# Performance work log

Measured on AMD Instinct MI355X. Metric: run time of the kernel, lower is better.

Reference implementation:

```python
import jax, jax.numpy as jnp
import numpy as np

B, D, H = 16384, 1024, 1024


def setup_inputs() -> dict:
    key = jax.random.key(0)
    ks = jax.random.split(key, 6)
    s = 1.0 / np.sqrt(D)
    return {
        "x": jax.random.normal(ks[0], (B, D), jnp.float32),
        "h_prev": jax.random.normal(ks[1], (B, H), jnp.float32),
        "c_prev": jax.random.normal(ks[2], (B, H), jnp.float32),
        "dynamic_weight": jax.random.uniform(ks[3], (B, H), jnp.float32),
        # stacked gate weights: order [i, f, o, c, s] along first axis
        "Wx": jax.random.normal(ks[4], (5 * H, D), jnp.float32) * s,
        "bx": jnp.zeros((5 * H,), jnp.float32),
        "Uh": jax.random.normal(ks[5], (5 * H, H), jnp.float32) * s,
        "bh": jnp.zeros((5 * H,), jnp.float32),
    }


def reference(x, h_prev, c_prev, dynamic_weight, Wx, bx, Uh, bh):
    # two fused GEMMs covering all 10 original nn.Linear calls
    gates = (jnp.einsum('bd,gd->bg', x, Wx) + bx
             + jnp.einsum('bh,gh->bg', h_prev, Uh) + bh)  # [B, 5H]
    gi, gf, go, gc, gs = jnp.split(gates, 5, axis=-1)
    i_t = jax.nn.sigmoid(gi)
    f_t = jax.nn.sigmoid(gf)
    o_t = jax.nn.sigmoid(go)
    c_hat = jnp.tanh(gc)
    s_t = jax.nn.sigmoid(gs) * dynamic_weight
    c_t = f_t * c_prev + i_t * c_hat * s_t
    h_t = o_t * jnp.tanh(c_t)
    return h_t, c_t
```

## Files before the change

kernel.cpp:

```cpp
#include <hip/hip_runtime.h>
#include <hip/hip_bf16.h>

#define B_ROWS 16384
#define KDIM   2048
#define NDIM   5120
#define HDIM   1024

#define BM 256
#define BN 256
#define BK 32
#define NK (KDIM / BK)
#define BUFSZ 32768
#define NBUF  4
#define LDS_BYTES (NBUF * BUFSZ)

typedef __attribute__((ext_vector_type(8))) short short8;
typedef __attribute__((ext_vector_type(4))) float f32x4;

__device__ __forceinline__ void async_cp16(const void* g, void* l) {
  __builtin_amdgcn_global_load_lds(
      (const __attribute__((address_space(1))) void*)g,
      (__attribute__((address_space(3))) void*)l,
      16, 0, 0);
}

__global__ void detect_dtype(const unsigned short* __restrict__ p, int* flag) {
  __shared__ int cnt;
  if (threadIdx.x == 0) cnt = 0;
  __syncthreads();
  int h = 0;
  for (int i = threadIdx.x; i < 2048; i += 256) {
    int e = (p[i] >> 7) & 0xFF;
    if (e >= 137) h++;
  }
  atomicAdd(&cnt, h);
  __syncthreads();
  if (threadIdx.x == 0) *flag = (cnt >= 4) ? 1 : 0;
}

__global__ void pack_pair_f32(const float* __restrict__ s0, const float* __restrict__ s1,
                              __hip_bfloat16* __restrict__ dst, const int* __restrict__ flag,
                              long rbase, long total) {
  if (*flag == 0) return;
  long idx = ((long)blockIdx.x * blockDim.x + threadIdx.x) * 8;
  if (idx >= total) return;
  int  k = (int)(idx & (KDIM - 1));
  long r = (idx >> 11) + rbase;
  const float* s = (k < 1024) ? (s0 + r * 1024 + k) : (s1 + r * 1024 + (k - 1024));
  float4 v0 = ((const float4*)s)[0];
  float4 v1 = ((const float4*)s)[1];
  union { short8 v; __hip_bfloat16 e[8]; } u;
  u.e[0] = __float2bfloat16(v0.x); u.e[1] = __float2bfloat16(v0.y);
  u.e[2] = __float2bfloat16(v0.z); u.e[3] = __float2bfloat16(v0.w);
  u.e[4] = __float2bfloat16(v1.x); u.e[5] = __float2bfloat16(v1.y);
  u.e[6] = __float2bfloat16(v1.z); u.e[7] = __float2bfloat16(v1.w);
  *(short8*)(dst + idx) = u.v;
}

__global__ __launch_bounds__(512, 2) void gemm_bt256(
    const __hip_bfloat16* __restrict__ Abf, const __hip_bfloat16* __restrict__ Wbf,
    const void* __restrict__ xr, const void* __restrict__ hr,
    const void* __restrict__ Wxr, const void* __restrict__ Uhr,
    __hip_bfloat16* __restrict__ G, const int* __restrict__ flag, int row_base) {
  extern __shared__ char lds[];

  const int tid = threadIdx.x;
  const int w   = tid >> 6;
  const int l   = tid & 63;

  const int m0l = blockIdx.y * BM;
  const int n0  = blockIdx.x * BN;

  const int wm = w >> 2;
  const int wn = w & 3;

  const int fl = *flag;
  const __hip_bfloat16* pA[2];
  const __hip_bfloat16* pW[2];
  long dA, dW;
  {
    const int r0 = w * 32 + (l >> 2);
#pragma unroll
    for (int i = 0; i < 2; ++i) {
      const int sr = r0 + i * 16;
      const int dc = (l & 3) ^ ((sr >> 1) & 3);
      if (fl) {
        pA[i] = Abf + (long)(m0l + sr) * KDIM + dc * 8;
        pW[i] = Wbf + (long)(n0 + sr) * KDIM + dc * 8;
      } else {
        pA[i] = (const __hip_bfloat16*)xr  + (long)(row_base + m0l + sr) * 1024 + dc * 8;
        pW[i] = (const __hip_bfloat16*)Wxr + (long)(n0 + sr) * 1024 + dc * 8;
      }
    }
    if (fl) { dA = 1024; dW = 1024; }
    else {
      dA = (const __hip_bfloat16*)hr  - (const __hip_bfloat16*)xr;
      dW = (const __hip_bfloat16*)Uhr - (const __hip_bfloat16*)Wxr;
    }
  }

#define STAGE(T) do {                                                        \
    const int  b_  = (T) & 3;                                                \
    const int  k0_ = (T) * BK;                                               \
    const long ko_ = (k0_ < 1024) ? (long)k0_ : (dA + (k0_ - 1024));         \
    const long kw_ = (k0_ < 1024) ? (long)k0_ : (dW + (k0_ - 1024));         \
    char* la_ = lds + b_ * BUFSZ + w * 2048;                                 \
    char* lw_ = la_ + 16384;                                                 \
    _Pragma("unroll")                                                        \
    for (int i_ = 0; i_ < 2; ++i_) {                                         \
      async_cp16(pA[i_] + ko_, la_ + i_ * 1024);                             \
      async_cp16(pW[i_] + kw_, lw_ + i_ * 1024);                             \
    }                                                                        \
  } while (0)

  f32x4 acc[8][4] = {};
  const int frow  = l & 15;
  const int swz   = (((l >> 4) ^ ((frow >> 1) & 3)) << 4);
  const int arow0 = wm * 128 + frow;
  const int brow0 = wn * 64 + frow;

#define COMPUTE(T) do {                                                      \
    const char* ba_ = lds + ((T) & 3) * BUFSZ;                               \
    const char* bw_ = ba_ + 16384;                                           \
    short8 af_[8], wf_[4];                                                   \
    _Pragma("unroll")                                                        \
    for (int mi = 0; mi < 8; ++mi)                                           \
      af_[mi] = *(const short8*)(ba_ + (arow0 + mi * 16) * 64 + swz);        \
    _Pragma("unroll")                                                        \
    for (int ni = 0; ni < 4; ++ni)                                           \
      wf_[ni] = *(const short8*)(bw_ + (brow0 + ni * 16) * 64 + swz);        \
    __builtin_amdgcn_s_setprio(1);                                           \
    _Pragma("unroll")                                                        \
    for (int mi = 0; mi < 8; ++mi)                                           \
      _Pragma("unroll")                                                      \
      for (int ni = 0; ni < 4; ++ni)                                         \
        acc[mi][ni] = __builtin_amdgcn_mfma_f32_16x16x32_bf16(               \
            af_[mi], wf_[ni], acc[mi][ni], 0, 0, 0);                         \
    __builtin_amdgcn_s_setprio(0);                                           \
  } while (0)

  STAGE(0); STAGE(1); STAGE(2);

  int t = 0;
  for (; t < NK - 3; ++t) {
    __builtin_amdgcn_s_barrier();
    __builtin_amdgcn_sched_barrier(0);
    STAGE(t + 3);
    asm volatile("s_waitcnt vmcnt(12)" ::: "memory");
    __builtin_amdgcn_s_barrier();
    __builtin_amdgcn_sched_barrier(0);
    COMPUTE(t);
  }
  for (; t < NK; ++t) {
    __builtin_amdgcn_s_barrier();
    __builtin_amdgcn_sched_barrier(0);
    asm volatile("s_waitcnt vmcnt(0)" ::: "memory");
    __builtin_amdgcn_s_barrier();
    __builtin_amdgcn_sched_barrier(0);
    COMPUTE(t);
  }

#undef STAGE
#undef COMPUTE

  const int c_col = l & 15;
  const int c_row = (l >> 4) * 4;
#pragma unroll
  for (int mi = 0; mi < 8; ++mi) {
#pragma unroll
    for (int r = 0; r < 4; ++r) {
      long m = (long)(m0l + wm * 128 + mi * 16 + c_row + r);
      __hip_bfloat16* gp = G + m * NDIM + n0 + wn * 64 + c_col;
#pragma unroll
      for (int ni = 0; ni < 4; ++ni)
        gp[ni * 16] = __float2bfloat16(acc[mi][ni][r]);
    }
  }
}

__global__ __launch_bounds__(256, 2) void gemm_bt128(
    const __hip_bfloat16* __restrict__ Abf, const __hip_bfloat16* __restrict__ Wbf,
    const void* __restrict__ xr, const void* __restrict__ hr,
    const void* __restrict__ Wxr, const void* __restrict__ Uhr,
    __hip_bfloat16* __restrict__ G, const int* __restrict__ flag, int row_base) {
  __shared__ __hip_bfloat16 As[128 * 64];
  __shared__ __hip_bfloat16 Ws[128 * 64];

  const int tid  = threadIdx.x;
  const int wave = tid >> 6;
  const int lane = tid & 63;

  const int m0l = blockIdx.y * 128;
  const int n0  = blockIdx.x * 128;

  const int wm = (wave >> 1) * 64;
  const int wn = (wave & 1) * 64;

  const int srl  = m0l + wave * 32 + (lane >> 3);
  const int srw  = n0  + wave * 32 + (lane >> 3);
  const int scol = (lane & 7) * 8;

  const int fl = *flag;
  const __hip_bfloat16 *pA0, *pA1, *pW0, *pW1;
  long rsA, rsW;
  if (fl) {
    pA0 = Abf + (long)srl * KDIM + scol; pA1 = pA0 + 1024; rsA = KDIM;
    pW0 = Wbf + (long)srw * KDIM + scol; pW1 = pW0 + 1024; rsW = KDIM;
  } else {
    pA0 = (const __hip_bfloat16*)xr  + (long)(row_base + srl) * 1024 + scol;
    pA1 = (const __hip_bfloat16*)hr  + (long)(row_base + srl) * 1024 + scol;
    pW0 = (const __hip_bfloat16*)Wxr + (long)srw * 1024 + scol;
    pW1 = (const __hip_bfloat16*)Uhr + (long)srw * 1024 + scol;
    rsA = 1024; rsW = 1024;
  }

  __hip_bfloat16* a_l = As + (wave * 32) * 64;
  __hip_bfloat16* w_l = Ws + (wave * 32) * 64;

  f32x4 acc[4][4] = {};
  const int frow = lane & 15;
  const int fk   = (lane >> 4) * 8;

  for (int k0 = 0; k0 < KDIM; k0 += 64) {
    const __hip_bfloat16* ag = (k0 < 1024) ? pA0 + k0 : pA1 + (k0 - 1024);
    const __hip_bfloat16* wg = (k0 < 1024) ? pW0 + k0 : pW1 + (k0 - 1024);
    __syncthreads();
#pragma unroll
    for (int i = 0; i < 4; ++i) {
      async_cp16(ag + (long)i * 8 * rsA, a_l + i * 8 * 64);
      async_cp16(wg + (long)i * 8 * rsW, w_l + i * 8 * 64);
    }
    __syncthreads();
#pragma unroll
    for (int kk = 0; kk < 64; kk += 32) {
      short8 af[4], wf[4];
#pragma unroll
      for (int mi = 0; mi < 4; ++mi)
        af[mi] = *(const short8*)(As + (wm + mi * 16 + frow) * 64 + kk + fk);
#pragma unroll
      for (int ni = 0; ni < 4; ++ni)
        wf[ni] = *(const short8*)(Ws + (wn + ni * 16 + frow) * 64 + kk + fk);
#pragma unroll
      for (int mi = 0; mi < 4; ++mi)
#pragma unroll
        for (int ni = 0; ni < 4; ++ni)
          acc[mi][ni] = __builtin_amdgcn_mfma_f32_16x16x32_bf16(
              af[mi], wf[ni], acc[mi][ni], 0, 0, 0);
    }
  }

  const int c_col = lane & 15;
  const int c_row = (lane >> 4) * 4;
#pragma unroll
  for (int mi = 0; mi < 4; ++mi) {
#pragma unroll
    for (int r = 0; r < 4; ++r) {
      long m = (long)(m0l + wm + mi * 16 + c_row + r);
      __hip_bfloat16* gp = G + m * NDIM + n0 + wn + c_col;
#pragma unroll
      for (int ni = 0; ni < 4; ++ni)
        gp[ni * 16] = __float2bfloat16(acc[mi][ni][r]);
    }
  }
}

__global__ void lstm_ep(const __hip_bfloat16* __restrict__ G,
                        const void* __restrict__ cpr, const void* __restrict__ dwr,
                        const void* __restrict__ bxr, const void* __restrict__ bhr,
                        float* __restrict__ out, const int* __restrict__ flag,
                        long row_base, long rows) {
  const long t = ((long)blockIdx.x * blockDim.x + threadIdx.x) * 8;
  if (t >= rows * HDIM) return;
  const long bl = t >> 10;
  const int  h  = (int)(t & 1023);
  const long ig = (row_base + bl) * HDIM + h;

  const int fl = *flag;
  const __hip_bfloat16* g = G + bl * (long)NDIM + h;

  union S8 { short8 v; __hip_bfloat16 e[8]; };
  union F8 { float4 v[2]; float f[8]; };

  S8 vg[5];
  F8 bias[5];
#pragma unroll
  for (int q = 0; q < 5; ++q) {
    vg[q].v = *(const short8*)(g + q * 1024);
    if (fl) {
      bias[q].v[0] = *(const float4*)((const float*)bxr + q * 1024 + h);
      bias[q].v[1] = *(const float4*)((const float*)bxr + q * 1024 + h + 4);
      F8 b2;
      b2.v[0] = *(const float4*)((const float*)bhr + q * 1024 + h);
      b2.v[1] = *(const float4*)((const float*)bhr + q * 1024 + h + 4);
#pragma unroll
      for (int j = 0; j < 8; ++j) bias[q].f[j] += b2.f[j];
    } else {
      S8 b1, b2;
      b1.v = *(const short8*)((const __hip_bfloat16*)bxr + q * 1024 + h);
      b2.v = *(const short8*)((const __hip_bfloat16*)bhr + q * 1024 + h);
#pragma unroll
      for (int j = 0; j < 8; ++j)
        bias[q].f[j] = __bfloat162float(b1.e[j]) + __bfloat162float(b2.e[j]);
    }
  }

  F8 cp, dv;
  if (fl) {
    cp.v[0] = *(const float4*)((const float*)cpr + ig);
    cp.v[1] = *(const float4*)((const float*)cpr + ig + 4);
    dv.v[0] = *(const float4*)((const float*)dwr + ig);
    dv.v[1] = *(const float4*)((const float*)dwr + ig + 4);
  } else {
    S8 c8, d8;
    c8.v = *(const short8*)((const __hip_bfloat16*)cpr + ig);
    d8.v = *(const short8*)((const __hip_bfloat16*)dwr + ig);
#pragma unroll
    for (int j = 0; j < 8; ++j) {
      cp.f[j] = __bfloat162float(c8.e[j]);
      dv.f[j] = __bfloat162float(d8.e[j]);
    }
  }

  F8 oh, oc;
#pragma unroll
  for (int j = 0; j < 8; ++j) {
    float gi = __bfloat162float(vg[0].e[j]) + bias[0].f[j];
    float gf = __bfloat162float(vg[1].e[j]) + bias[1].f[j];
    float go = __bfloat162float(vg[2].e[j]) + bias[2].f[j];
    float gc = __bfloat162float(vg[3].e[j]) + bias[3].f[j];
    float gs = __bfloat162float(vg[4].e[j]) + bias[4].f[j];
    float it = 1.f / (1.f + __expf(-gi));
    float ft = 1.f / (1.f + __expf(-gf));
    float ot = 1.f / (1.f + __expf(-go));
    float ch = tanhf(gc);
    float st = (1.f / (1.f + __expf(-gs))) * dv.f[j];
    float ct = ft * cp.f[j] + it * ch * st;
    oh.f[j] = ot * tanhf(ct);
    oc.f[j] = ct;
  }
  *(float4*)(out + ig)     = oh.v[0];
  *(float4*)(out + ig + 4) = oh.v[1];
  float* oc_p = out + (long)B_ROWS * HDIM + ig;
  *(float4*)(oc_p)     = oc.v[0];
  *(float4*)(oc_p + 4) = oc.v[1];
}

extern "C" void kernel_launch(void* const* d_in, const int* in_sizes, int n_in,
                              void* d_out, int out_size, void* d_ws, size_t ws_size,
                              hipStream_t stream) {
  const void* x      = d_in[0];
  const void* h_prev = d_in[1];
  const void* c_prev = d_in[2];
  const void* dw     = d_in[3];
  const void* Wx     = d_in[4];
  const void* bx     = d_in[5];
  const void* Uh     = d_in[6];
  const void* bh     = d_in[7];

  static int lds_attr_done = 0;
  if (!lds_attr_done) {
    hipFuncSetAttribute((const void*)gemm_bt256,
                        hipFuncAttributeMaxDynamicSharedMemorySize, LDS_BYTES);
    lds_attr_done = 1;
  }

  const size_t wbf_bytes = (size_t)NDIM * KDIM * 2;
  int nc = 32;
  for (int c = 1; c <= 32; c <<= 1) {
    size_t need = 256 + wbf_bytes
                + (size_t)(B_ROWS / c) * KDIM * 2
                + (size_t)(B_ROWS / c) * NDIM * 2;
    if (need <= ws_size) { nc = c; break; }
  }
  const long rows = B_ROWS / nc;

  char* ws = (char*)d_ws;
  int* flag = (int*)ws;
  __hip_bfloat16* Wbf = (__hip_bfloat16*)(ws + 256);
  __hip_bfloat16* Abf = (__hip_bfloat16*)(ws + 256 + wbf_bytes);
  __hip_bfloat16* G   = (__hip_bfloat16*)(ws + 256 + wbf_bytes + (size_t)rows * KDIM * 2);

  detect_dtype<<<1, 256, 0, stream>>>((const unsigned short*)x, flag);

  pack_pair_f32<<<(int)(((long)NDIM * KDIM) / 2048), 256, 0, stream>>>(
      (const float*)Wx, (const float*)Uh, Wbf, flag, 0, (long)NDIM * KDIM);

  const bool use256 = (rows >= 4096);

  for (int c = 0; c < nc; ++c) {
    long rbase = c * rows;
    pack_pair_f32<<<(int)rows, 256, 0, stream>>>(
        (const float*)x, (const float*)h_prev, Abf, flag, rbase, rows * KDIM);
    if (use256) {
      dim3 grid(NDIM / BN, (int)(rows / BM));
      gemm_bt256<<<grid, 512, LDS_BYTES, stream>>>(
          Abf, Wbf, x, h_prev, Wx, Uh, G, flag, (int)rbase);
    } else {
      dim3 grid(NDIM / 128, (int)(rows / 128));
      gemm_bt128<<<grid, 256, 0, stream>>>(
          Abf, Wbf, x, h_prev, Wx, Uh, G, flag, (int)rbase);
    }
    lstm_ep<<<(int)(rows * HDIM / 2048), 256, 0, stream>>>(
        G, c_prev, dw, bx, bh, (float*)d_out, flag, rbase, rows);
  }
}
```

Before: 719.5 us.

## Fuse LSTM gate epilogue into GEMM with gate-interleaved 256x320 tiles

Each GEMM tile now holds all five gate columns for the same 64 hidden units (N tile of 320, gate-interleaved weight rows), so the LSTM pointwise math runs directly on the accumulators. This removes the bf16 gate buffer G, its write and re-read, and the separate epilogue kernel, and it also shrinks the workspace need so fewer row chunks may be used. In exchange the K step grows to 64 with only double buffering, which leaves less prefetch depth. Accumulators grow to 8x5 fragments, raising register pressure, and the epilogue does scalar strided loads and stores of c_prev, dynamic_weight and the outputs.

After: 681.6 us. 5.3% less time.

```diff
diff --git a/kernel.cpp b/kernel.cpp
--- a/kernel.cpp
+++ b/kernel.cpp
@@ -7,12 +7,13 @@
 #define HDIM   1024
 
 #define BM 256
-#define BN 256
-#define BK 32
-#define NK (KDIM / BK)
-#define BUFSZ 32768
-#define NBUF  4
-#define LDS_BYTES (NBUF * BUFSZ)
+#define BN 320
+#define BK 64
+#define NKT (KDIM / BK)
+#define A_BYTES (BM * BK * 2)
+#define W_BYTES (BN * BK * 2)
+#define BUFSZ   (A_BYTES + W_BYTES)
+#define LDS_BYTES (2 * BUFSZ)
 
 typedef __attribute__((ext_vector_type(8))) short short8;
 typedef __attribute__((ext_vector_type(4))) float f32x4;
@@ -57,11 +58,13 @@
   *(short8*)(dst + idx) = u.v;
 }
 
-__global__ __launch_bounds__(512, 2) void gemm_bt256(
+__global__ __launch_bounds__(512, 2) void gemm_fused(
     const __hip_bfloat16* __restrict__ Abf, const __hip_bfloat16* __restrict__ Wbf,
     const void* __restrict__ xr, const void* __restrict__ hr,
     const void* __restrict__ Wxr, const void* __restrict__ Uhr,
-    __hip_bfloat16* __restrict__ G, const int* __restrict__ flag, int row_base) {
+    const void* __restrict__ cpr, const void* __restrict__ dwr,
+    const void* __restrict__ bxr, const void* __restrict__ bhr,
+    float* __restrict__ out, const int* __restrict__ flag, int row_base) {
   extern __shared__ char lds[];
 
   const int tid = threadIdx.x;
@@ -69,280 +72,155 @@
   const int l   = tid & 63;
 
   const int m0l = blockIdx.y * BM;
-  const int n0  = blockIdx.x * BN;
+  const int h0  = blockIdx.x * 64;
 
   const int wm = w >> 2;
   const int wn = w & 3;
 
   const int fl = *flag;
-  const __hip_bfloat16* pA[2];
-  const __hip_bfloat16* pW[2];
-  long dA, dW;
+  const int dc = (l & 7) ^ (l >> 3);
+
+  const __hip_bfloat16* srcA;
+  long strA, dA;
+  if (fl) {
+    srcA = Abf + (long)(m0l + w * 8 + (l >> 3)) * KDIM + dc * 8;
+    strA = KDIM; dA = 1024;
+  } else {
+    srcA = (const __hip_bfloat16*)xr
+         + (long)(row_base + m0l + w * 8 + (l >> 3)) * 1024 + dc * 8;
+    strA = 1024;
+    dA = (const __hip_bfloat16*)hr - (const __hip_bfloat16*)xr;
+  }
+
+  const __hip_bfloat16* srcW[5];
+  long dW;
   {
-    const int r0 = w * 32 + (l >> 2);
-#pragma unroll
-    for (int i = 0; i < 2; ++i) {
-      const int sr = r0 + i * 16;
-      const int dc = (l & 3) ^ ((sr >> 1) & 3);
-      if (fl) {
-        pA[i] = Abf + (long)(m0l + sr) * KDIM + dc * 8;
-        pW[i] = Wbf + (long)(n0 + sr) * KDIM + dc * 8;
-      } else {
-        pA[i] = (const __hip_bfloat16*)xr  + (long)(row_base + m0l + sr) * 1024 + dc * 8;
-        pW[i] = (const __hip_bfloat16*)Wxr + (long)(n0 + sr) * 1024 + dc * 8;
-      }
-    }
-    if (fl) { dA = 1024; dW = 1024; }
+    const __hip_bfloat16* wbase;
+    long strW;
+    if (fl) { wbase = Wbf; strW = KDIM; dW = 1024; }
     else {
-      dA = (const __hip_bfloat16*)hr  - (const __hip_bfloat16*)xr;
+      wbase = (const __hip_bfloat16*)Wxr; strW = 1024;
       dW = (const __hip_bfloat16*)Uhr - (const __hip_bfloat16*)Wxr;
     }
+#pragma unroll
+    for (int i = 0; i < 5; ++i) {
+      const int j  = w + i * 8;
+      const int wg = j / 10;
+      const int q  = j % 10;
+      const int g  = q >> 1;
+      const int hs = (q & 1) * 8 + (l >> 3);
+      const long r_w = (long)g * 1024 + h0 + wg * 16 + hs;
+      srcW[i] = wbase + r_w * strW + dc * 8;
+    }
   }
 
 #define STAGE(T) do {                                                        \
-    const int  b_  = (T) & 3;                                                \
+    const int  b_  = (T) & 1;                                                \
     const int  k0_ = (T) * BK;                                               \
-    const long ko_ = (k0_ < 1024) ? (long)k0_ : (dA + (k0_ - 1024));         \
-    const long kw_ = (k0_ < 1024) ? (long)k0_ : (dW + (k0_ - 1024));         \
-    char* la_ = lds + b_ * BUFSZ + w * 2048;                                 \
-    char* lw_ = la_ + 16384;                                                 \
+    const long koA_ = (k0_ < 1024) ? (long)k0_ : (dA + (k0_ - 1024));        \
+    const long koW_ = (k0_ < 1024) ? (long)k0_ : (dW + (k0_ - 1024));        \
+    char* lb_ = lds + b_ * BUFSZ;                                            \
     _Pragma("unroll")                                                        \
-    for (int i_ = 0; i_ < 2; ++i_) {                                         \
-      async_cp16(pA[i_] + ko_, la_ + i_ * 1024);                             \
-      async_cp16(pW[i_] + kw_, lw_ + i_ * 1024);                             \
+    for (int i_ = 0; i_ < 4; ++i_)                                           \
+      async_cp16(srcA + koA_ + (long)i_ * 64 * strA,                         \
+                 lb_ + (w + i_ * 8) * 1024 + l * 16);                        \
+    _Pragma("unroll")                                                        \
+    for (int i_ = 0; i_ < 5; ++i_)                                           \
+      async_cp16(srcW[i_] + koW_,                                            \
+                 lb_ + A_BYTES + (w + i_ * 8) * 1024 + l * 16);              \
+  } while (0)
+
+  f32x4 acc[8][5] = {};
+  const int frow = l & 15;
+  const int aoff0 = (wm * 128 + frow) * 128;
+  const int woff0 = A_BYTES + (wn * 80 + frow) * 128;
+
+#define COMPUTE(T) do {                                                      \
+    const char* ba_ = lds + ((T) & 1) * BUFSZ;                               \
+    _Pragma("unroll")                                                        \
+    for (int kk = 0; kk < 2; ++kk) {                                         \
+      const int sc_ = ((kk * 4 + (l >> 4)) ^ (l & 7)) * 16;                  \
+      short8 wf_[5], af_[8];                                                 \
+      _Pragma("unroll")                                                      \
+      for (int nj = 0; nj < 5; ++nj)                                         \
+        wf_[nj] = *(const short8*)(ba_ + woff0 + nj * 2048 + sc_);           \
+      _Pragma("unroll")                                                      \
+      for (int mi = 0; mi < 8; ++mi)                                         \
+        af_[mi] = *(const short8*)(ba_ + aoff0 + mi * 2048 + sc_);           \
+      __builtin_amdgcn_s_setprio(1);                                         \
+      _Pragma("unroll")                                                      \
+      for (int mi = 0; mi < 8; ++mi)                                         \
+        _Pragma("unroll")                                                    \
+        for (int nj = 0; nj < 5; ++nj)                                       \
+          acc[mi][nj] = __builtin_amdgcn_mfma_f32_16x16x32_bf16(             \
+              af_[mi], wf_[nj], acc[mi][nj], 0, 0, 0);                       \
+      __builtin_amdgcn_s_setprio(0);                                         \
     }                                                                        \
   } while (0)
 
-  f32x4 acc[8][4] = {};
-  const int frow  = l & 15;
-  const int swz   = (((l >> 4) ^ ((frow >> 1) & 3)) << 4);
-  const int arow0 = wm * 128 + frow;
-  const int brow0 = wn * 64 + frow;
-
-#define COMPUTE(T) do {                                                      \
-    const char* ba_ = lds + ((T) & 3) * BUFSZ;                               \
-    const char* bw_ = ba_ + 16384;                                           \
-    short8 af_[8], wf_[4];                                                   \
-    _Pragma("unroll")                                                        \
-    for (int mi = 0; mi < 8; ++mi)                                           \
-      af_[mi] = *(const short8*)(ba_ + (arow0 + mi * 16) * 64 + swz);        \
-    _Pragma("unroll")                                                        \
-    for (int ni = 0; ni < 4; ++ni)                                           \
-      wf_[ni] = *(const short8*)(bw_ + (brow0 + ni * 16) * 64 + swz);        \
-    __builtin_amdgcn_s_setprio(1);                                           \
-    _Pragma("unroll")                                                        \
-    for (int mi = 0; mi < 8; ++mi)                                           \
-      _Pragma("unroll")                                                      \
-      for (int ni = 0; ni < 4; ++ni)                                         \
-        acc[mi][ni] = __builtin_amdgcn_mfma_f32_16x16x32_bf16(               \
-            af_[mi], wf_[ni], acc[mi][ni], 0, 0, 0);                         \
-    __builtin_amdgcn_s_setprio(0);                                           \
-  } while (0)
-
-  STAGE(0); STAGE(1); STAGE(2);
-
-  int t = 0;
-  for (; t < NK - 3; ++t) {
+  STAGE(0);
+
+  for (int t = 0; t < NKT - 1; ++t) {
     __builtin_amdgcn_s_barrier();
     __builtin_amdgcn_sched_barrier(0);
-    STAGE(t + 3);
-    asm volatile("s_waitcnt vmcnt(12)" ::: "memory");
+    STAGE(t + 1);
+    asm volatile("s_waitcnt vmcnt(9)" ::: "memory");
+    __builtin_amdgcn_sched_barrier(0);
     __builtin_amdgcn_s_barrier();
     __builtin_amdgcn_sched_barrier(0);
     COMPUTE(t);
   }
-  for (; t < NK; ++t) {
-    __builtin_amdgcn_s_barrier();
-    __builtin_amdgcn_sched_barrier(0);
-    asm volatile("s_waitcnt vmcnt(0)" ::: "memory");
-    __builtin_amdgcn_s_barrier();
-    __builtin_amdgcn_sched_barrier(0);
-    COMPUTE(t);
-  }
+  __builtin_amdgcn_s_barrier();
+  asm volatile("s_waitcnt vmcnt(0)" ::: "memory");
+  __builtin_amdgcn_sched_barrier(0);
+  __builtin_amdgcn_s_barrier();
+  __builtin_amdgcn_sched_barrier(0);
+  COMPUTE(NKT - 1);
 
 #undef STAGE
 #undef COMPUTE
 
-  const int c_col = l & 15;
-  const int c_row = (l >> 4) * 4;
+  const int hh = h0 + wn * 16 + frow;
+  float bsum[5];
+#pragma unroll
+  for (int g = 0; g < 5; ++g) {
+    if (fl) {
+      bsum[g] = ((const float*)bxr)[g * 1024 + hh] + ((const float*)bhr)[g * 1024 + hh];
+    } else {
+      bsum[g] = __bfloat162float(((const __hip_bfloat16*)bxr)[g * 1024 + hh])
+              + __bfloat162float(((const __hip_bfloat16*)bhr)[g * 1024 + hh]);
+    }
+  }
+  const long orow0 = (long)row_base + m0l + wm * 128 + (l >> 4) * 4;
+  float* outc = out + (long)B_ROWS * HDIM;
 #pragma unroll
   for (int mi = 0; mi < 8; ++mi) {
 #pragma unroll
     for (int r = 0; r < 4; ++r) {
-      long m = (long)(m0l + wm * 128 + mi * 16 + c_row + r);
-      __hip_bfloat16* gp = G + m * NDIM + n0 + wn * 64 + c_col;
-#pragma unroll
-      for (int ni = 0; ni < 4; ++ni)
-        gp[ni * 16] = __float2bfloat16(acc[mi][ni][r]);
-    }
-  }
-}
-
-__global__ __launch_bounds__(256, 2) void gemm_bt128(
-    const __hip_bfloat16* __restrict__ Abf, const __hip_bfloat16* __restrict__ Wbf,
-    const void* __restrict__ xr, const void* __restrict__ hr,
-    const void* __restrict__ Wxr, const void* __restrict__ Uhr,
-    __hip_bfloat16* __restrict__ G, const int* __restrict__ flag, int row_base) {
-  __shared__ __hip_bfloat16 As[128 * 64];
-  __shared__ __hip_bfloat16 Ws[128 * 64];
-
-  const int tid  = threadIdx.x;
-  const int wave = tid >> 6;
-  const int lane = tid & 63;
-
-  const int m0l = blockIdx.y * 128;
-  const int n0  = blockIdx.x * 128;
-
-  const int wm = (wave >> 1) * 64;
-  const int wn = (wave & 1) * 64;
-
-  const int srl  = m0l + wave * 32 + (lane >> 3);
-  const int srw  = n0  + wave * 32 + (lane >> 3);
-  const int scol = (lane & 7) * 8;
-
-  const int fl = *flag;
-  const __hip_bfloat16 *pA0, *pA1, *pW0, *pW1;
-  long rsA, rsW;
-  if (fl) {
-    pA0 = Abf + (long)srl * KDIM + scol; pA1 = pA0 + 1024; rsA = KDIM;
-    pW0 = Wbf + (long)srw * KDIM + scol; pW1 = pW0 + 1024; rsW = KDIM;
-  } else {
-    pA0 = (const __hip_bfloat16*)xr  + (long)(row_base + srl) * 1024 + scol;
-    pA1 = (const __hip_bfloat16*)hr  + (long)(row_base + srl) * 1024 + scol;
-    pW0 = (const __hip_bfloat16*)Wxr + (long)srw * 1024 + scol;
-    pW1 = (const __hip_bfloat16*)Uhr + (long)srw * 1024 + scol;
-    rsA = 1024; rsW = 1024;
-  }
-
-  __hip_bfloat16* a_l = As + (wave * 32) * 64;
-  __hip_bfloat16* w_l = Ws + (wave * 32) * 64;
-
-  f32x4 acc[4][4] = {};
-  const int frow = lane & 15;
-  const int fk   = (lane >> 4) * 8;
-
-  for (int k0 = 0; k0 < KDIM; k0 += 64) {
-    const __hip_bfloat16* ag = (k0 < 1024) ? pA0 + k0 : pA1 + (k0 - 1024);
-    const __hip_bfloat16* wg = (k0 < 1024) ? pW0 + k0 : pW1 + (k0 - 1024);
-    __syncthreads();
-#pragma unroll
-    for (int i = 0; i < 4; ++i) {
-      async_cp16(ag + (long)i * 8 * rsA, a_l + i * 8 * 64);
-      async_cp16(wg + (long)i * 8 * rsW, w_l + i * 8 * 64);
-    }
-    __syncthreads();
-#pragma unroll
-    for (int kk = 0; kk < 64; kk += 32) {
-      short8 af[4], wf[4];
-#pragma unroll
-      for (int mi = 0; mi < 4; ++mi)
-        af[mi] = *(const short8*)(As + (wm + mi * 16 + frow) * 64 + kk + fk);
-#pragma unroll
-      for (int ni = 0; ni < 4; ++ni)
-        wf[ni] = *(const short8*)(Ws + (wn + ni * 16 + frow) * 64 + kk + fk);
-#pragma unroll
-      for (int mi = 0; mi < 4; ++mi)
-#pragma unroll
-        for (int ni = 0; ni < 4; ++ni)
-          acc[mi][ni] = __builtin_amdgcn_mfma_f32_16x16x32_bf16(
-              af[mi], wf[ni], acc[mi][ni], 0, 0, 0);
-    }
-  }
-
-  const int c_col = lane & 15;
-  const int c_row = (lane >> 4) * 4;
-#pragma unroll
-  for (int mi = 0; mi < 4; ++mi) {
-#pragma unroll
-    for (int r = 0; r < 4; ++r) {
-      long m = (long)(m0l + wm + mi * 16 + c_row + r);
-      __hip_bfloat16* gp = G + m * NDIM + n0 + wn + c_col;
-#pragma unroll
-      for (int ni = 0; ni < 4; ++ni)
-        gp[ni * 16] = __float2bfloat16(acc[mi][ni][r]);
-    }
-  }
-}
-
-__global__ void lstm_ep(const __hip_bfloat16* __restrict__ G,
-                        const void* __restrict__ cpr, const void* __restrict__ dwr,
-                        const void* __restrict__ bxr, const void* __restrict__ bhr,
-                        float* __restrict__ out, const int* __restrict__ flag,
-                        long row_base, long rows) {
-  const long t = ((long)blockIdx.x * blockDim.x + threadIdx.x) * 8;
-  if (t >= rows * HDIM) return;
-  const long bl = t >> 10;
-  const int  h  = (int)(t & 1023);
-  const long ig = (row_base + bl) * HDIM + h;
-
-  const int fl = *flag;
-  const __hip_bfloat16* g = G + bl * (long)NDIM + h;
-
-  union S8 { short8 v; __hip_bfloat16 e[8]; };
-  union F8 { float4 v[2]; float f[8]; };
-
-  S8 vg[5];
-  F8 bias[5];
-#pragma unroll
-  for (int q = 0; q < 5; ++q) {
-    vg[q].v = *(const short8*)(g + q * 1024);
-    if (fl) {
-      bias[q].v[0] = *(const float4*)((const float*)bxr + q * 1024 + h);
-      bias[q].v[1] = *(const float4*)((const float*)bxr + q * 1024 + h + 4);
-      F8 b2;
-      b2.v[0] = *(const float4*)((const float*)bhr + q * 1024 + h);
-      b2.v[1] = *(const float4*)((const float*)bhr + q * 1024 + h + 4);
-#pragma unroll
-      for (int j = 0; j < 8; ++j) bias[q].f[j] += b2.f[j];
-    } else {
-      S8 b1, b2;
-      b1.v = *(const short8*)((const __hip_bfloat16*)bxr + q * 1024 + h);
-      b2.v = *(const short8*)((const __hip_bfloat16*)bhr + q * 1024 + h);
-#pragma unroll
-      for (int j = 0; j < 8; ++j)
-        bias[q].f[j] = __bfloat162float(b1.e[j]) + __bfloat162float(b2.e[j]);
-    }
-  }
-
-  F8 cp, dv;
-  if (fl) {
-    cp.v[0] = *(const float4*)((const float*)cpr + ig);
-    cp.v[1] = *(const float4*)((const float*)cpr + ig + 4);
-    dv.v[0] = *(const float4*)((const float*)dwr + ig);
-    dv.v[1] = *(const float4*)((const float*)dwr + ig + 4);
-  } else {
-    S8 c8, d8;
-    c8.v = *(const short8*)((const __hip_bfloat16*)cpr + ig);
-    d8.v = *(const short8*)((const __hip_bfloat16*)dwr + ig);
-#pragma unroll
-    for (int j = 0; j < 8; ++j) {
-      cp.f[j] = __bfloat162float(c8.e[j]);
-      dv.f[j] = __bfloat162float(d8.e[j]);
-    }
-  }
-
-  F8 oh, oc;
-#pragma unroll
-  for (int j = 0; j < 8; ++j) {
-    float gi = __bfloat162float(vg[0].e[j]) + bias[0].f[j];
-    float gf = __bfloat162float(vg[1].e[j]) + bias[1].f[j];
-    float go = __bfloat162float(vg[2].e[j]) + bias[2].f[j];
-    float gc = __bfloat162float(vg[3].e[j]) + bias[3].f[j];
-    float gs = __bfloat162float(vg[4].e[j]) + bias[4].f[j];
-    float it = 1.f / (1.f + __expf(-gi));
-    float ft = 1.f / (1.f + __expf(-gf));
-    float ot = 1.f / (1.f + __expf(-go));
-    float ch = tanhf(gc);
-    float st = (1.f / (1.f + __expf(-gs))) * dv.f[j];
-    float ct = ft * cp.f[j] + it * ch * st;
-    oh.f[j] = ot * tanhf(ct);
-    oc.f[j] = ct;
-  }
-  *(float4*)(out + ig)     = oh.v[0];
-  *(float4*)(out + ig + 4) = oh.v[1];
-  float* oc_p = out + (long)B_ROWS * HDIM + ig;
-  *(float4*)(oc_p)     = oc.v[0];
-  *(float4*)(oc_p + 4) = oc.v[1];
+      const long idx = (orow0 + mi * 16 + r) * HDIM + hh;
+      float cp, dv;
+      if (fl) {
+        cp = ((const float*)cpr)[idx];
+        dv = ((const float*)dwr)[idx];
+      } else {
+        cp = __bfloat162float(((const __hip_bfloat16*)cpr)[idx]);
+        dv = __bfloat162float(((const __hip_bfloat16*)dwr)[idx]);
+      }
+      const float gi = acc[mi][0][r] + bsum[0];
+      const float gf = acc[mi][1][r] + bsum[1];
+      const float go = acc[mi][2][r] + bsum[2];
+      const float gc = acc[mi][3][r] + bsum[3];
+      const float gs = acc[mi][4][r] + bsum[4];
+      const float it = 1.f / (1.f + __expf(-gi));
+      const float ft = 1.f / (1.f + __expf(-gf));
+      const float ot = 1.f / (1.f + __expf(-go));
+      const float ch = tanhf(gc);
+      const float st = (1.f / (1.f + __expf(-gs))) * dv;
+      const float ct = ft * cp + it * ch * st;
+      out[idx]  = ot * tanhf(ct);
+      outc[idx] = ct;
+    }
+  }
 }
 
 extern "C" void kernel_launch(void* const* d_in, const int* in_sizes, int n_in,
@@ -359,7 +237,7 @@
 
   static int lds_attr_done = 0;
   if (!lds_attr_done) {
-    hipFuncSetAttribute((const void*)gemm_bt256,
+    hipFuncSetAttribute((const void*)gemm_fused,
                         hipFuncAttributeMaxDynamicSharedMemorySize, LDS_BYTES);
     lds_attr_done = 1;
   }
@@ -368,8 +246,7 @@
   int nc = 32;
   for (int c = 1; c <= 32; c <<= 1) {
     size_t need = 256 + wbf_bytes
-                + (size_t)(B_ROWS / c) * KDIM * 2
-                + (size_t)(B_ROWS / c) * NDIM * 2;
+                + (size_t)(B_ROWS / c) * KDIM * 2;
     if (need <= ws_size) { nc = c; break; }
   }
   const long rows = B_ROWS / nc;
@@ -378,29 +255,19 @@
   int* flag = (int*)ws;
   __hip_bfloat16* Wbf = (__hip_bfloat16*)(ws + 256);
   __hip_bfloat16* Abf = (__hip_bfloat16*)(ws + 256 + wbf_bytes);
-  __hip_bfloat16* G   = (__hip_bfloat16*)(ws + 256 + wbf_bytes + (size_t)rows * KDIM * 2);
 
   detect_dtype<<<1, 256, 0, stream>>>((const unsigned short*)x, flag);
 
   pack_pair_f32<<<(int)(((long)NDIM * KDIM) / 2048), 256, 0, stream>>>(
       (const float*)Wx, (const float*)Uh, Wbf, flag, 0, (long)NDIM * KDIM);
-
-  const bool use256 = (rows >= 4096);
 
   for (int c = 0; c < nc; ++c) {
     long rbase = c * rows;
     pack_pair_f32<<<(int)rows, 256, 0, stream>>>(
         (const float*)x, (const float*)h_prev, Abf, flag, rbase, rows * KDIM);
-    if (use256) {
-      dim3 grid(NDIM / BN, (int)(rows / BM));
-      gemm_bt256<<<grid, 512, LDS_BYTES, stream>>>(
-          Abf, Wbf, x, h_prev, Wx, Uh, G, flag, (int)rbase);
-    } else {
-      dim3 grid(NDIM / 128, (int)(rows / 128));
-      gemm_bt128<<<grid, 256, 0, stream>>>(
-          Abf, Wbf, x, h_prev, Wx, Uh, G, flag, (int)rbase);
-    }
-    lstm_ep<<<(int)(rows * HDIM / 2048), 256, 0, stream>>>(
-        G, c_prev, dw, bx, bh, (float*)d_out, flag, rbase, rows);
-  }
-}
+    dim3 grid(NDIM / BN, (int)(rows / BM));
+    gemm_fused<<<grid, 512, LDS_BYTES, stream>>>(
+        Abf, Wbf, x, h_prev, Wx, Uh, c_prev, dw, bx, bh,
+        (float*)d_out, flag, (int)rbase);
+  }
+}
```
